# Kernel optimization log

Hardware: AMD Instinct MI355X
Metric: run time of the kernel (lower is better)

Reference implementation:

```python
import jax, jax.numpy as jnp
import numpy as np

N = 50000      # num_nodes
R = 8          # num_relations
FIN = 128      # in_channels
H = 128        # hidden_channels
E = 800000     # num_edges (avg degree 16)


def _xavier(key, shape):
    fan_in, fan_out = shape[-2], shape[-1]
    lim = np.sqrt(6.0 / (fan_in + fan_out)).astype(np.float32)
    return jax.random.uniform(key, shape, jnp.float32, -lim, lim)


def setup_inputs() -> dict:
    key = jax.random.key(0)
    ks = jax.random.split(key, 10)
    return {
        "x": jax.random.normal(ks[0], (N, FIN), jnp.float32),
        "edge_index": jax.random.randint(ks[1], (2, E), 0, N, jnp.int32),
        "edge_type": jax.random.randint(ks[2], (E,), 0, R, jnp.int32),
        "rel_w0": _xavier(ks[3], (R, FIN, H)),
        "root_w0": _xavier(ks[4], (FIN, H)),
        "bias0": jnp.zeros((H,), jnp.float32),
        "rel_w1": _xavier(ks[5], (R, H, H)),
        "root_w1": _xavier(ks[6], (H, H)),
        "bias1": jnp.zeros((H,), jnp.float32),
        "rel_emb": _xavier(ks[7], (R, H)),
    }


def _rgcn_conv(x, src, dst, etype, rel_w, root_w, bias):
    # RGCNConv (PyG, aggr='mean'): out_i = root(x_i) + sum_r W_r * mean_{j in N_r(i)} x_j
    n = x.shape[0]
    seg = dst * R + etype                                   # fused (node, relation) segment id
    msgs = x[src]                                           # [E, F] gather
    sums = jax.ops.segment_sum(msgs, seg, num_segments=n * R)
    cnt = jax.ops.segment_sum(jnp.ones((src.shape[0], 1), x.dtype), seg, num_segments=n * R)
    mean = (sums / jnp.maximum(cnt, 1.0)).reshape(n, R, -1)  # [N, R, F]
    return jnp.einsum('nrf,rfh->nh', mean, rel_w) + x @ root_w + bias


def reference(x, edge_index, edge_type, rel_w0, root_w0, bias0,
              rel_w1, root_w1, bias1, rel_emb):
    src, dst = edge_index[0], edge_index[1]
    h = _rgcn_conv(x, src, dst, edge_type, rel_w0, root_w0, bias0)
    h = jax.nn.relu(h)  # dropout in eval mode (identity)
    h = _rgcn_conv(h, src, dst, edge_type, rel_w1, root_w1, bias1)
    return (h, rel_emb)
```

## Files before the change

kernel.cpp:

```cpp
#include <hip/hip_runtime.h>

typedef unsigned short ushort_t;
typedef __attribute__((ext_vector_type(8))) short short8;
typedef __attribute__((ext_vector_type(4))) float f32x4;
typedef __attribute__((ext_vector_type(4))) int int4v;

#define RNUM 8
#define FDIM 128
#define KDIM 1152

__device__ __forceinline__ float bf2f(ushort_t u) {
    union { unsigned int i; float f; } x;
    x.i = ((unsigned int)u) << 16;
    return x.f;
}
__device__ __forceinline__ ushort_t f2bf(float f) {
    union { float f; unsigned int i; } x;
    x.f = f;
    unsigned int u = x.i;
    u += 0x7fffu + ((u >> 16) & 1u);
    return (ushort_t)(u >> 16);
}

__device__ __forceinline__ void gl_lds16(const void* g, void* s) {
    __builtin_amdgcn_global_load_lds(
        (const __attribute__((address_space(1))) unsigned int*)g,
        (__attribute__((address_space(3))) unsigned int*)s, 16, 0, 0);
}


__global__ void init_head(int* __restrict__ head, int n) {
    int i = blockIdx.x * 256 + threadIdx.x;
    if (i < n) head[i] = -1;
}

__global__ void link_kernel(const int* __restrict__ dst, const int* __restrict__ et,
                            int* head, int* __restrict__ nxt, int E) {
    int i = blockIdx.x * 256 + threadIdx.x;
    if (i < E) {
        int seg = dst[i] * RNUM + et[i];
        nxt[i] = atomicExch(&head[seg], i);
    }
}


__global__ __launch_bounds__(256) void transpose_w(const float* __restrict__ rel_w,
                                                   const float* __restrict__ root_w,
                                                   ushort_t* __restrict__ Wt) {
    int r = blockIdx.x;
    const float* src = (r < 8) ? (rel_w + r * 16384) : root_w;
    __shared__ ushort_t t[128 * 130];
    for (int idx = threadIdx.x; idx < 16384; idx += 256)
        t[(idx >> 7) * 130 + (idx & 127)] = f2bf(src[idx]);
    __syncthreads();
    ushort_t* d = Wt + r * 16384;
    for (int idx = threadIdx.x; idx < 16384; idx += 256)
        d[idx] = t[(idx & 127) * 130 + (idx >> 7)];
}


__global__ void cast_x(const float* __restrict__ x, ushort_t* __restrict__ Mx, int total) {
    int i = (blockIdx.x * 256 + threadIdx.x) * 8;
    if (i >= total) return;
    float4 v0 = *(const float4*)(x + i);
    float4 v1 = *(const float4*)(x + i + 4);
    ushort_t o[8] = {f2bf(v0.x), f2bf(v0.y), f2bf(v0.z), f2bf(v0.w),
                     f2bf(v1.x), f2bf(v1.y), f2bf(v1.z), f2bf(v1.w)};
    int row = i >> 7, col = i & 127;
    *(int4v*)(Mx + (size_t)row * KDIM + 1024 + col) = *(int4v*)o;
}


__global__ __launch_bounds__(256) void seg_mean(const int* __restrict__ head,
                                                const int* __restrict__ nxt,
                                                const int* __restrict__ esrc,
                                                ushort_t* Mx, int NSEG) {
    int t = blockIdx.x * 256 + threadIdx.x;
    int g = t >> 4;
    int l16 = t & 15;
    int segBase = g * 4;
    if (segBase >= NSEG) return;
    const ushort_t* gbase = Mx + 1024 + (size_t)l16 * 8;

    float acc[4][8];
    int cnt[4];
    int j[4], s[4], nx[4];
#pragma unroll
    for (int c = 0; c < 4; ++c) {
        cnt[c] = 0;
#pragma unroll
        for (int k = 0; k < 8; ++k) acc[c][k] = 0.f;
        int sg = segBase + c;
        j[c] = (sg < NSEG) ? head[sg] : -1;
    }
#pragma unroll
    for (int c = 0; c < 4; ++c)
        if (j[c] >= 0) { s[c] = esrc[j[c]]; nx[c] = nxt[j[c]]; }

    while ((j[0] & j[1] & j[2] & j[3]) >= 0) {
        int4v v[4];
#pragma unroll
        for (int c = 0; c < 4; ++c)
            if (j[c] >= 0) v[c] = *(const int4v*)(gbase + (size_t)s[c] * KDIM);
        int s2[4], nx2[4];
#pragma unroll
        for (int c = 0; c < 4; ++c)
            if (j[c] >= 0 && nx[c] >= 0) { s2[c] = esrc[nx[c]]; nx2[c] = nxt[nx[c]]; }
#pragma unroll
        for (int c = 0; c < 4; ++c) {
            if (j[c] >= 0) {
                const ushort_t* p = (const ushort_t*)&v[c];
#pragma unroll
                for (int k = 0; k < 8; ++k) acc[c][k] += bf2f(p[k]);
                ++cnt[c];
                j[c] = nx[c];
                s[c] = s2[c];
                nx[c] = nx2[c];
            }
        }
    }

#pragma unroll
    for (int c = 0; c < 4; ++c) {
        int sg = segBase + c;
        if (sg < NSEG) {
            float sc = (cnt[c] > 0) ? 1.0f / (float)cnt[c] : 0.f;
            ushort_t ov[8];
#pragma unroll
            for (int k = 0; k < 8; ++k) ov[k] = f2bf(acc[c][k] * sc);
            *(int4v*)(Mx + (size_t)(sg >> 3) * KDIM + (sg & 7) * 128 + l16 * 8) = *(int4v*)ov;
        }
    }
}


template <bool FINAL>
__global__ __launch_bounds__(256) void rgcn_gemm(
    const ushort_t* Mx, const ushort_t* __restrict__ Wt,
    const float* __restrict__ bias, float* __restrict__ outF,
    ushort_t* MxOut, int N) {
    __shared__ ushort_t As[128 * 128];
    __shared__ ushort_t Bs[128 * 128];
    int tid = threadIdx.x;
    int wid = tid >> 6, lane = tid & 63;
    int l16 = lane & 15, q = lane >> 4;
    int nodeBase = blockIdx.x * 128;

    f32x4 acc[2][8];
#pragma unroll
    for (int rt = 0; rt < 2; ++rt)
#pragma unroll
        for (int ct = 0; ct < 8; ++ct) acc[rt][ct] = (f32x4){0.f, 0.f, 0.f, 0.f};

    for (int r = 0; r < 9; ++r) {
        __syncthreads();
#pragma unroll
        for (int i = 0; i < 8; ++i) {
            int L = i * 256 + tid;
            int row = L >> 4;
            int c = (L & 15) ^ (row & 15);
            gl_lds16(Mx + (size_t)(nodeBase + row) * KDIM + r * 128 + c * 8,
                     (char*)As + (size_t)L * 16);
            gl_lds16(Wt + r * 16384 + row * 128 + c * 8,
                     (char*)Bs + (size_t)L * 16);
        }
        __syncthreads();
#pragma unroll
        for (int s = 0; s < 4; ++s) {
            int pos = ((s * 4 + q) ^ l16) * 16;
            short8 a0 = *(const short8*)((const char*)As + ((2 * wid + 0) * 16 + l16) * 256 + pos);
            short8 a1 = *(const short8*)((const char*)As + ((2 * wid + 1) * 16 + l16) * 256 + pos);
#pragma unroll
            for (int ct = 0; ct < 8; ++ct) {
                short8 b = *(const short8*)((const char*)Bs + (ct * 16 + l16) * 256 + pos);
                acc[0][ct] = __builtin_amdgcn_mfma_f32_16x16x32_bf16(a0, b, acc[0][ct], 0, 0, 0);
                acc[1][ct] = __builtin_amdgcn_mfma_f32_16x16x32_bf16(a1, b, acc[1][ct], 0, 0, 0);
            }
        }
    }
#pragma unroll
    for (int rt = 0; rt < 2; ++rt) {
#pragma unroll
        for (int ct = 0; ct < 8; ++ct) {
            int h = ct * 16 + l16;
            float bv = bias[h];
#pragma unroll
            for (int reg = 0; reg < 4; ++reg) {
                int node = nodeBase + (2 * wid + rt) * 16 + q * 4 + reg;
                if (node < N) {
                    float v = acc[rt][ct][reg] + bv;
                    if (FINAL) {
                        outF[(size_t)node * FDIM + h] = v;
                    } else {
                        v = fmaxf(v, 0.f);
                        MxOut[(size_t)node * KDIM + 1024 + h] = f2bf(v);
                    }
                }
            }
        }
    }
}

__global__ void copy_emb(const float* __restrict__ e, float* __restrict__ out, int n) {
    int i = blockIdx.x * 256 + threadIdx.x;
    if (i < n) out[i] = e[i];
}


extern "C" void kernel_launch(void* const* d_in, const int* in_sizes, int n_in,
                              void* d_out, int out_size, void* d_ws, size_t ws_size,
                              hipStream_t stream) {
    const float* x        = (const float*)d_in[0];
    const int* edge_index = (const int*)d_in[1];
    const int* edge_type  = (const int*)d_in[2];
    const float* rel_w0   = (const float*)d_in[3];
    const float* root_w0  = (const float*)d_in[4];
    const float* bias0    = (const float*)d_in[5];
    const float* rel_w1   = (const float*)d_in[6];
    const float* root_w1  = (const float*)d_in[7];
    const float* bias1    = (const float*)d_in[8];
    const float* rel_emb  = (const float*)d_in[9];

    int N = in_sizes[0] / FDIM;
    int E = in_sizes[1] / 2;
    int NSEG = N * RNUM;
    const int* src = edge_index;
    const int* dst = edge_index + E;

    int nb_gemm = (N + 127) / 128;
    int NPAD = nb_gemm * 128;

    char* w = (char*)d_ws;
    auto alloc = [&](size_t bytes) -> char* {
        char* p = w;
        w += (bytes + 255) & ~(size_t)255;
        return p;
    };
    int* head    = (int*)alloc((size_t)NSEG * 4);
    int* nxt     = (int*)alloc((size_t)E * 4);
    ushort_t* Wt = (ushort_t*)alloc((size_t)2 * 9 * 16384 * 2);
    ushort_t* Mx = (ushort_t*)alloc((size_t)NPAD * KDIM * 2);
    (void)ws_size; (void)n_in; (void)out_size;

    int nb_seg  = (NSEG + 255) / 256;
    int nb_E    = (E + 255) / 256;
    int ngrp    = (NSEG + 3) / 4;
    int nb_mean = (ngrp * 16 + 255) / 256;
    int nb_cast = (N * FDIM) / (256 * 8);

    init_head<<<nb_seg, 256, 0, stream>>>(head, NSEG);
    link_kernel<<<nb_E, 256, 0, stream>>>(dst, edge_type, head, nxt, E);
    transpose_w<<<9, 256, 0, stream>>>(rel_w0, root_w0, Wt);
    transpose_w<<<9, 256, 0, stream>>>(rel_w1, root_w1, Wt + 9 * 16384);
    cast_x<<<nb_cast, 256, 0, stream>>>(x, Mx, N * FDIM);

    seg_mean<<<nb_mean, 256, 0, stream>>>(head, nxt, src, Mx, NSEG);
    rgcn_gemm<false><<<nb_gemm, 256, 0, stream>>>(Mx, Wt, bias0, nullptr, Mx, N);
    seg_mean<<<nb_mean, 256, 0, stream>>>(head, nxt, src, Mx, NSEG);
    rgcn_gemm<true><<<nb_gemm, 256, 0, stream>>>(Mx, Wt + 9 * 16384, bias1,
                                                 (float*)d_out, nullptr, N);
    copy_emb<<<4, 256, 0, stream>>>(rel_emb, (float*)d_out + (size_t)N * FDIM,
                                    in_sizes[9]);
}
```

Baseline: 353.5 us.

## Fuse segment-mean gather into GEMM, computing relation means directly in LDS

Gathering of per-relation neighbor means now happens inside the GEMM kernel, which writes each relation's bf16 mean tile straight into shared memory instead of staging a wide [N,1152] buffer in global memory. Edge source and next pointer are packed into a single int2 array so each linked-list step needs one load, and block size grows to 512 threads with one 16-row tile per wave. This removes the global write and re-read of the 9x-wide aggregation matrix and two kernel launches, at the cost of only 391 blocks whose gathers are latency-bound and serialized with the MFMA work per relation.

```diff
diff --git a/kernel.cpp b/kernel.cpp
--- a/kernel.cpp
+++ b/kernel.cpp
@@ -7,7 +7,6 @@
 
 #define RNUM 8
 #define FDIM 128
-#define KDIM 1152
 
 __device__ __forceinline__ float bf2f(ushort_t u) {
     union { unsigned int i; float f; } x;
@@ -34,12 +33,14 @@
     if (i < n) head[i] = -1;
 }
 
-__global__ void link_kernel(const int* __restrict__ dst, const int* __restrict__ et,
-                            int* head, int* __restrict__ nxt, int E) {
+__global__ void link_kernel(const int* __restrict__ src, const int* __restrict__ dst,
+                            const int* __restrict__ et,
+                            int* head, int2* __restrict__ meta, int E) {
     int i = blockIdx.x * 256 + threadIdx.x;
     if (i < E) {
         int seg = dst[i] * RNUM + et[i];
-        nxt[i] = atomicExch(&head[seg], i);
+        int prev = atomicExch(&head[seg], i);
+        meta[i] = make_int2(src[i], prev);
     }
 }
 
@@ -59,143 +60,138 @@
 }
 
 
-__global__ void cast_x(const float* __restrict__ x, ushort_t* __restrict__ Mx, int total) {
+__global__ void cast_x(const float* __restrict__ x, ushort_t* __restrict__ xc,
+                       int total, int totalPad) {
     int i = (blockIdx.x * 256 + threadIdx.x) * 8;
-    if (i >= total) return;
-    float4 v0 = *(const float4*)(x + i);
-    float4 v1 = *(const float4*)(x + i + 4);
-    ushort_t o[8] = {f2bf(v0.x), f2bf(v0.y), f2bf(v0.z), f2bf(v0.w),
-                     f2bf(v1.x), f2bf(v1.y), f2bf(v1.z), f2bf(v1.w)};
-    int row = i >> 7, col = i & 127;
-    *(int4v*)(Mx + (size_t)row * KDIM + 1024 + col) = *(int4v*)o;
-}
-
-
-__global__ __launch_bounds__(256) void seg_mean(const int* __restrict__ head,
-                                                const int* __restrict__ nxt,
-                                                const int* __restrict__ esrc,
-                                                ushort_t* Mx, int NSEG) {
-    int t = blockIdx.x * 256 + threadIdx.x;
-    int g = t >> 4;
-    int l16 = t & 15;
-    int segBase = g * 4;
-    if (segBase >= NSEG) return;
-    const ushort_t* gbase = Mx + 1024 + (size_t)l16 * 8;
-
-    float acc[4][8];
-    int cnt[4];
-    int j[4], s[4], nx[4];
-#pragma unroll
-    for (int c = 0; c < 4; ++c) {
-        cnt[c] = 0;
-#pragma unroll
-        for (int k = 0; k < 8; ++k) acc[c][k] = 0.f;
-        int sg = segBase + c;
-        j[c] = (sg < NSEG) ? head[sg] : -1;
-    }
-#pragma unroll
-    for (int c = 0; c < 4; ++c)
-        if (j[c] >= 0) { s[c] = esrc[j[c]]; nx[c] = nxt[j[c]]; }
-
-    while ((j[0] & j[1] & j[2] & j[3]) >= 0) {
-        int4v v[4];
-#pragma unroll
-        for (int c = 0; c < 4; ++c)
-            if (j[c] >= 0) v[c] = *(const int4v*)(gbase + (size_t)s[c] * KDIM);
-        int s2[4], nx2[4];
-#pragma unroll
-        for (int c = 0; c < 4; ++c)
-            if (j[c] >= 0 && nx[c] >= 0) { s2[c] = esrc[nx[c]]; nx2[c] = nxt[nx[c]]; }
-#pragma unroll
-        for (int c = 0; c < 4; ++c) {
-            if (j[c] >= 0) {
-                const ushort_t* p = (const ushort_t*)&v[c];
-#pragma unroll
-                for (int k = 0; k < 8; ++k) acc[c][k] += bf2f(p[k]);
-                ++cnt[c];
-                j[c] = nx[c];
-                s[c] = s2[c];
-                nx[c] = nx2[c];
-            }
-        }
-    }
-
-#pragma unroll
-    for (int c = 0; c < 4; ++c) {
-        int sg = segBase + c;
-        if (sg < NSEG) {
-            float sc = (cnt[c] > 0) ? 1.0f / (float)cnt[c] : 0.f;
-            ushort_t ov[8];
-#pragma unroll
-            for (int k = 0; k < 8; ++k) ov[k] = f2bf(acc[c][k] * sc);
-            *(int4v*)(Mx + (size_t)(sg >> 3) * KDIM + (sg & 7) * 128 + l16 * 8) = *(int4v*)ov;
-        }
-    }
+    if (i >= totalPad) return;
+    ushort_t o[8];
+    if (i < total) {
+        float4 v0 = *(const float4*)(x + i);
+        float4 v1 = *(const float4*)(x + i + 4);
+        o[0] = f2bf(v0.x); o[1] = f2bf(v0.y); o[2] = f2bf(v0.z); o[3] = f2bf(v0.w);
+        o[4] = f2bf(v1.x); o[5] = f2bf(v1.y); o[6] = f2bf(v1.z); o[7] = f2bf(v1.w);
+    } else {
+#pragma unroll
+        for (int k = 0; k < 8; ++k) o[k] = 0;
+    }
+    *(int4v*)(xc + i) = *(int4v*)o;
 }
 
 
 template <bool FINAL>
-__global__ __launch_bounds__(256) void rgcn_gemm(
-    const ushort_t* Mx, const ushort_t* __restrict__ Wt,
-    const float* __restrict__ bias, float* __restrict__ outF,
-    ushort_t* MxOut, int N) {
+__global__ __launch_bounds__(512, 4) void rgcn_fused(
+    const int* __restrict__ head, const int2* __restrict__ meta,
+    const ushort_t* __restrict__ X,
+    const ushort_t* __restrict__ Wt,
+    const float* __restrict__ bias,
+    float* __restrict__ outF, ushort_t* __restrict__ Xout, int N) {
     __shared__ ushort_t As[128 * 128];
     __shared__ ushort_t Bs[128 * 128];
+    __shared__ int headL[128 * RNUM];
     int tid = threadIdx.x;
-    int wid = tid >> 6, lane = tid & 63;
+    int wv = tid >> 6, lane = tid & 63;
     int l16 = lane & 15, q = lane >> 4;
+    int qw = tid >> 4;
     int nodeBase = blockIdx.x * 128;
 
-    f32x4 acc[2][8];
-#pragma unroll
-    for (int rt = 0; rt < 2; ++rt)
-#pragma unroll
-        for (int ct = 0; ct < 8; ++ct) acc[rt][ct] = (f32x4){0.f, 0.f, 0.f, 0.f};
+    for (int i = tid; i < 128 * RNUM; i += 512)
+        headL[i] = (nodeBase + (i >> 3) < N) ? head[nodeBase * RNUM + i] : -1;
+
+    f32x4 acc[8];
+#pragma unroll
+    for (int ct = 0; ct < 8; ++ct) acc[ct] = (f32x4){0.f, 0.f, 0.f, 0.f};
+
+    __syncthreads();
 
     for (int r = 0; r < 9; ++r) {
-        __syncthreads();
-#pragma unroll
-        for (int i = 0; i < 8; ++i) {
-            int L = i * 256 + tid;
+        if (r > 0) __syncthreads();
+        if (r < 8) {
+            int row0 = qw * 4;
+            float av[4][8];
+            int ccnt[4], cj[4], cs[4], cn[4];
+#pragma unroll
+            for (int c = 0; c < 4; ++c) {
+                ccnt[c] = 0;
+#pragma unroll
+                for (int k = 0; k < 8; ++k) av[c][k] = 0.f;
+                cj[c] = headL[(row0 + c) * RNUM + r];
+            }
+#pragma unroll
+            for (int c = 0; c < 4; ++c)
+                if (cj[c] >= 0) { int2 m = meta[cj[c]]; cs[c] = m.x; cn[c] = m.y; }
+            while ((cj[0] & cj[1] & cj[2] & cj[3]) >= 0) {
+                int4v v[4];
+#pragma unroll
+                for (int c = 0; c < 4; ++c)
+                    if (cj[c] >= 0) v[c] = *(const int4v*)(X + (size_t)cs[c] * FDIM + l16 * 8);
+                int2 m2[4];
+#pragma unroll
+                for (int c = 0; c < 4; ++c)
+                    if (cj[c] >= 0 && cn[c] >= 0) m2[c] = meta[cn[c]];
+#pragma unroll
+                for (int c = 0; c < 4; ++c) {
+                    if (cj[c] >= 0) {
+                        const ushort_t* p = (const ushort_t*)&v[c];
+#pragma unroll
+                        for (int k = 0; k < 8; ++k) av[c][k] += bf2f(p[k]);
+                        ++ccnt[c];
+                        cj[c] = cn[c];
+                        cs[c] = m2[c].x;
+                        cn[c] = m2[c].y;
+                    }
+                }
+            }
+#pragma unroll
+            for (int c = 0; c < 4; ++c) {
+                int row = row0 + c;
+                float sc = (ccnt[c] > 0) ? 1.0f / (float)ccnt[c] : 0.f;
+                ushort_t ov[8];
+#pragma unroll
+                for (int k = 0; k < 8; ++k) ov[k] = f2bf(av[c][k] * sc);
+                *(int4v*)((char*)As + row * 256 + ((l16 ^ (row & 15)) * 16)) = *(int4v*)ov;
+            }
+        } else {
+#pragma unroll
+            for (int i = 0; i < 4; ++i) {
+                int L = i * 512 + tid;
+                int row = L >> 4;
+                int c = (L & 15) ^ (row & 15);
+                gl_lds16(X + (size_t)(nodeBase + row) * FDIM + c * 8,
+                         (char*)As + (size_t)L * 16);
+            }
+        }
+#pragma unroll
+        for (int i = 0; i < 4; ++i) {
+            int L = i * 512 + tid;
             int row = L >> 4;
             int c = (L & 15) ^ (row & 15);
-            gl_lds16(Mx + (size_t)(nodeBase + row) * KDIM + r * 128 + c * 8,
-                     (char*)As + (size_t)L * 16);
-            gl_lds16(Wt + r * 16384 + row * 128 + c * 8,
-                     (char*)Bs + (size_t)L * 16);
+            gl_lds16(Wt + r * 16384 + row * 128 + c * 8, (char*)Bs + (size_t)L * 16);
         }
         __syncthreads();
 #pragma unroll
         for (int s = 0; s < 4; ++s) {
             int pos = ((s * 4 + q) ^ l16) * 16;
-            short8 a0 = *(const short8*)((const char*)As + ((2 * wid + 0) * 16 + l16) * 256 + pos);
-            short8 a1 = *(const short8*)((const char*)As + ((2 * wid + 1) * 16 + l16) * 256 + pos);
+            short8 a = *(const short8*)((const char*)As + (wv * 16 + l16) * 256 + pos);
 #pragma unroll
             for (int ct = 0; ct < 8; ++ct) {
                 short8 b = *(const short8*)((const char*)Bs + (ct * 16 + l16) * 256 + pos);
-                acc[0][ct] = __builtin_amdgcn_mfma_f32_16x16x32_bf16(a0, b, acc[0][ct], 0, 0, 0);
-                acc[1][ct] = __builtin_amdgcn_mfma_f32_16x16x32_bf16(a1, b, acc[1][ct], 0, 0, 0);
-            }
-        }
-    }
-#pragma unroll
-    for (int rt = 0; rt < 2; ++rt) {
-#pragma unroll
-        for (int ct = 0; ct < 8; ++ct) {
-            int h = ct * 16 + l16;
-            float bv = bias[h];
-#pragma unroll
-            for (int reg = 0; reg < 4; ++reg) {
-                int node = nodeBase + (2 * wid + rt) * 16 + q * 4 + reg;
-                if (node < N) {
-                    float v = acc[rt][ct][reg] + bv;
-                    if (FINAL) {
-                        outF[(size_t)node * FDIM + h] = v;
-                    } else {
-                        v = fmaxf(v, 0.f);
-                        MxOut[(size_t)node * KDIM + 1024 + h] = f2bf(v);
-                    }
-                }
+                acc[ct] = __builtin_amdgcn_mfma_f32_16x16x32_bf16(a, b, acc[ct], 0, 0, 0);
+            }
+        }
+    }
+
+#pragma unroll
+    for (int ct = 0; ct < 8; ++ct) {
+        int h = ct * 16 + l16;
+        float bv = bias[h];
+#pragma unroll
+        for (int reg = 0; reg < 4; ++reg) {
+            int node = nodeBase + wv * 16 + q * 4 + reg;
+            float v = acc[ct][reg] + bv;
+            if (FINAL) {
+                if (node < N) outF[(size_t)node * FDIM + h] = v;
+            } else {
+                Xout[(size_t)node * FDIM + h] = f2bf(fmaxf(v, 0.f));
             }
         }
     }
@@ -236,29 +232,27 @@
         w += (bytes + 255) & ~(size_t)255;
         return p;
     };
-    int* head    = (int*)alloc((size_t)NSEG * 4);
-    int* nxt     = (int*)alloc((size_t)E * 4);
-    ushort_t* Wt = (ushort_t*)alloc((size_t)2 * 9 * 16384 * 2);
-    ushort_t* Mx = (ushort_t*)alloc((size_t)NPAD * KDIM * 2);
+    int* head     = (int*)alloc((size_t)NSEG * 4);
+    int2* meta    = (int2*)alloc((size_t)E * 8);
+    ushort_t* Wt  = (ushort_t*)alloc((size_t)2 * 9 * 16384 * 2);
+    ushort_t* xc  = (ushort_t*)alloc((size_t)NPAD * FDIM * 2);
+    ushort_t* h1c = (ushort_t*)alloc((size_t)NPAD * FDIM * 2);
     (void)ws_size; (void)n_in; (void)out_size;
 
     int nb_seg  = (NSEG + 255) / 256;
     int nb_E    = (E + 255) / 256;
-    int ngrp    = (NSEG + 3) / 4;
-    int nb_mean = (ngrp * 16 + 255) / 256;
-    int nb_cast = (N * FDIM) / (256 * 8);
+    int nb_cast = (NPAD * FDIM) / (256 * 8);
 
     init_head<<<nb_seg, 256, 0, stream>>>(head, NSEG);
-    link_kernel<<<nb_E, 256, 0, stream>>>(dst, edge_type, head, nxt, E);
+    link_kernel<<<nb_E, 256, 0, stream>>>(src, dst, edge_type, head, meta, E);
     transpose_w<<<9, 256, 0, stream>>>(rel_w0, root_w0, Wt);
     transpose_w<<<9, 256, 0, stream>>>(rel_w1, root_w1, Wt + 9 * 16384);
-    cast_x<<<nb_cast, 256, 0, stream>>>(x, Mx, N * FDIM);
-
-    seg_mean<<<nb_mean, 256, 0, stream>>>(head, nxt, src, Mx, NSEG);
-    rgcn_gemm<false><<<nb_gemm, 256, 0, stream>>>(Mx, Wt, bias0, nullptr, Mx, N);
-    seg_mean<<<nb_mean, 256, 0, stream>>>(head, nxt, src, Mx, NSEG);
-    rgcn_gemm<true><<<nb_gemm, 256, 0, stream>>>(Mx, Wt + 9 * 16384, bias1,
-                                                 (float*)d_out, nullptr, N);
+    cast_x<<<nb_cast, 256, 0, stream>>>(x, xc, N * FDIM, NPAD * FDIM);
+
+    rgcn_fused<false><<<nb_gemm, 512, 0, stream>>>(head, meta, xc, Wt, bias0,
+                                                   nullptr, h1c, N);
+    rgcn_fused<true><<<nb_gemm, 512, 0, stream>>>(head, meta, h1c, Wt + 9 * 16384, bias1,
+                                                  (float*)d_out, nullptr, N);
     copy_emb<<<4, 256, 0, stream>>>(rel_emb, (float*)d_out + (size_t)N * FDIM,
                                     in_sizes[9]);
 }
```

Result: slower. 393.9 us (+11.4%).
